# Kernel tuning notes

Measured on AMD Instinct MI355X. Metric: run time of the kernel, lower is better.

Reference implementation:

```python
import jax, jax.numpy as jnp
import numpy as np

N_NODES = 50000
N_EDGES = 1_600_000
IN_C, HID_C, OUT_C = 512, 256, 50
ALPHA = 0.1
NUM_LAYERS = 10


def setup_inputs() -> dict:
    key = jax.random.key(0)
    ks = jax.random.split(key, 8)
    x = jax.random.normal(ks[0], (N_NODES, IN_C), dtype=jnp.float32)
    edge_row = jax.random.randint(ks[1], (N_EDGES,), 0, N_NODES, dtype=jnp.int32)
    edge_col = jax.random.randint(ks[2], (N_EDGES,), 0, N_NODES, dtype=jnp.int32)
    edge_weight = jax.random.uniform(ks[3], (N_EDGES,), dtype=jnp.float32)
    s1 = 1.0 / np.sqrt(IN_C)
    s2 = 1.0 / np.sqrt(HID_C)
    W1 = jax.random.uniform(ks[4], (IN_C, HID_C), minval=-s1, maxval=s1, dtype=jnp.float32)
    b1 = jax.random.uniform(ks[5], (HID_C,), minval=-s1, maxval=s1, dtype=jnp.float32)
    W2 = jax.random.uniform(ks[6], (HID_C, OUT_C), minval=-s2, maxval=s2, dtype=jnp.float32)
    b2 = jax.random.uniform(ks[7], (OUT_C,), minval=-s2, maxval=s2, dtype=jnp.float32)
    return {"x": x, "edge_row": edge_row, "edge_col": edge_col,
            "edge_weight": edge_weight, "W1": W1, "b1": b1, "W2": W2, "b2": b2}


def reference(x, edge_row, edge_col, edge_weight, W1, b1, W2, b2):
    # MLP: Linear -> ReLU -> Linear (dropout inactive in eval, no batch norm)
    h = jax.nn.relu(x @ W1 + b1)          # [N, HID_C]
    h = h @ W2 + b2                        # [N, OUT_C]
    x0 = h

    def spmm(v):
        # out[i] = sum_{e: row[e]==i} w[e] * v[col[e]]
        msgs = v[edge_col] * edge_weight[:, None]   # [E, OUT_C]
        return jax.ops.segment_sum(msgs, edge_row, num_segments=N_NODES)

    def step(h, _):
        h = spmm(h) * (1.0 - ALPHA) + ALPHA * x0
        return h, None

    h, _ = jax.lax.scan(step, h, None, length=NUM_LAYERS)
    return jax.nn.log_softmax(h, axis=1)
```

## Files before the change

kernel.cpp:

```cpp
#include <hip/hip_runtime.h>
#include <cstddef>
#include <cstdint>
#include <math.h>

#define N_NODES 50000
#define N_EDGES 1600000
#define IN_C 512
#define HID_C 256
#define OUT_C 50
#define PAD_C 64
#define NUM_LAYERS 10
#define NBUCK 98
#define BSHIFT 9
#define BCAP 20480
#define PHB_CHUNK 8192
#define PHB_BLOCKS 196

typedef __attribute__((ext_vector_type(8))) short short8;
typedef __attribute__((ext_vector_type(4))) float floatx4;

__device__ inline unsigned short f2bf(float f) {
    unsigned int u = __float_as_uint(f);
    u += 0x7fffu + ((u >> 16) & 1u);
    return (unsigned short)(u >> 16);
}

#define ASYNC16(g, l)                                                     \
    __builtin_amdgcn_global_load_lds(                                     \
        (const __attribute__((address_space(1))) void*)(g),               \
        (__attribute__((address_space(3))) void*)(l), 16, 0, 0)

#define WAITCNT6() asm volatile("s_waitcnt vmcnt(6)" ::: "memory")
#define WAITCNT0() asm volatile("s_waitcnt vmcnt(0)" ::: "memory")
#define SBAR()     __builtin_amdgcn_s_barrier()
#define SFENCE()   __builtin_amdgcn_sched_barrier(0)

__global__ __launch_bounds__(256) void transpose_w1(const float* __restrict__ W1,
                                                    unsigned short* __restrict__ Wt) {
    __shared__ float tile[32][33];
    int bx = blockIdx.x;
    int by = blockIdx.y;
    int tx = threadIdx.x & 31, ty = threadIdx.x >> 5;
#pragma unroll
    for (int i = 0; i < 32; i += 8)
        tile[ty + i][tx] = W1[(bx * 32 + ty + i) * HID_C + by * 32 + tx];
    __syncthreads();
#pragma unroll
    for (int i = 0; i < 32; i += 8)
        Wt[(size_t)(by * 32 + ty + i) * IN_C + bx * 32 + tx] = f2bf(tile[tx][ty + i]);
}

__global__ void pad_w2(const float* __restrict__ W2, const float* __restrict__ b2,
                       unsigned short* __restrict__ Wpt, float* __restrict__ bp) {
    int idx = blockIdx.x * blockDim.x + threadIdx.x;
    if (idx < PAD_C * HID_C) {
        int n = idx >> 8, k = idx & 255;
        float v = (n < OUT_C) ? W2[k * OUT_C + n] : 0.f;
        Wpt[idx] = f2bf(v);
    }
    if (idx < PAD_C) bp[idx] = (idx < OUT_C) ? b2[idx] : 0.f;
}

__global__ __launch_bounds__(256) void gemm1_fused(const float* __restrict__ A,
                                                   const unsigned short* __restrict__ Wt,
                                                   const float* __restrict__ b1,
                                                   const unsigned short* __restrict__ Wpt,
                                                   const float* __restrict__ bp,
                                                   float* __restrict__ h0f,
                                                   unsigned short* __restrict__ h0b) {
    __shared__ __align__(16) char smem[49152];
    float*          As0 = (float*)smem;
    float*          As1 = (float*)(smem + 8192);
    unsigned short* Bs0 = (unsigned short*)(smem + 16384);
    unsigned short* Bs1 = (unsigned short*)(smem + 32768);
    unsigned short* Hs  = (unsigned short*)smem;
    const int HS_LD = 264;

    const int tid  = threadIdx.x;
    const int wave = tid >> 6, lane = tid & 63;
    const int quad = lane >> 4, l16 = lane & 15;
    const int m0 = blockIdx.x * 64;
    const int wm = (wave >> 1) * 32;
    const int wn = (wave & 1) * 128;

    floatx4 acc[2][8];
#pragma unroll
    for (int i = 0; i < 2; ++i)
#pragma unroll
        for (int j = 0; j < 8; ++j) acc[i][j] = (floatx4){0.f, 0.f, 0.f, 0.f};

    auto stage = [&](float* As_, unsigned short* Bs_, int k0) {
#pragma unroll
        for (int j = 0; j < 2; ++j) {
            int slot = tid + j * 256;
            int r = slot >> 3, c = slot & 7;
            int gr = m0 + r;
            if (gr >= N_NODES) gr = N_NODES - 1;
            const float* src = A + (size_t)gr * IN_C + k0 + ((c ^ (r & 7)) << 2);
            ASYNC16(src, As_ + (slot << 2));
        }
#pragma unroll
        for (int j = 0; j < 4; ++j) {
            const unsigned short* src = Wt + (size_t)tid * IN_C + k0 + (j << 3);
            ASYNC16(src, Bs_ + (j << 11) + (tid << 3));
        }
    };

    auto compute = [&](const float* As_, const unsigned short* Bs_) {
        short8 bfr[8], afr[2];
#pragma unroll
        for (int nt = 0; nt < 8; ++nt) {
            int n = wn + nt * 16 + l16;
            bfr[nt] = *(const short8*)&Bs_[(quad << 11) + (n << 3)];
        }
#pragma unroll
        for (int mt = 0; mt < 2; ++mt) {
            int r  = wm + mt * 16 + l16;
            int rx = r & 7;
            float4 lo = *(const float4*)&As_[(r << 5) + (((2 * quad)     ^ rx) << 2)];
            float4 hi = *(const float4*)&As_[(r << 5) + (((2 * quad + 1) ^ rx) << 2)];
            short8 a;
            a[0] = (short)f2bf(lo.x); a[1] = (short)f2bf(lo.y);
            a[2] = (short)f2bf(lo.z); a[3] = (short)f2bf(lo.w);
            a[4] = (short)f2bf(hi.x); a[5] = (short)f2bf(hi.y);
            a[6] = (short)f2bf(hi.z); a[7] = (short)f2bf(hi.w);
            afr[mt] = a;
        }
#pragma unroll
        for (int mt = 0; mt < 2; ++mt)
#pragma unroll
            for (int nt = 0; nt < 8; ++nt)
                acc[mt][nt] = __builtin_amdgcn_mfma_f32_16x16x32_bf16(afr[mt], bfr[nt],
                                                                      acc[mt][nt], 0, 0, 0);
    };

    stage(As0, Bs0, 0);
    stage(As1, Bs1, 32);
    WAITCNT6(); SFENCE(); SBAR(); SFENCE();
    for (int kk = 0; kk < 7; ++kk) {
        compute(As0, Bs0);
        SFENCE(); SBAR(); SFENCE();
        stage(As0, Bs0, (2 * kk + 2) * 32);
        WAITCNT6(); SFENCE(); SBAR(); SFENCE();
        compute(As1, Bs1);
        SFENCE(); SBAR(); SFENCE();
        stage(As1, Bs1, (2 * kk + 3) * 32);
        WAITCNT6(); SFENCE(); SBAR(); SFENCE();
    }
    compute(As0, Bs0);
    SFENCE(); SBAR(); SFENCE();
    WAITCNT0(); SFENCE(); SBAR(); SFENCE();
    compute(As1, Bs1);
    __syncthreads();

#pragma unroll
    for (int nt = 0; nt < 8; ++nt) {
        int n = wn + nt * 16 + l16;
        float bn = b1[n];
#pragma unroll
        for (int mt = 0; mt < 2; ++mt)
#pragma unroll
            for (int r = 0; r < 4; ++r) {
                float v = acc[mt][nt][r] + bn;
                v = v > 0.f ? v : 0.f;
                Hs[(wm + mt * 16 + quad * 4 + r) * HS_LD + n] = f2bf(v);
            }
    }
    __syncthreads();

    floatx4 acc2[4];
#pragma unroll
    for (int nt = 0; nt < 4; ++nt) acc2[nt] = (floatx4){0.f, 0.f, 0.f, 0.f};
    const int hrow = (wave << 4) + l16;
#pragma unroll
    for (int k2 = 0; k2 < 8; ++k2) {
        short8 haf = *(const short8*)&Hs[hrow * HS_LD + (k2 << 5) + (quad << 3)];
#pragma unroll
        for (int nt = 0; nt < 4; ++nt) {
            short8 bf = *(const short8*)&Wpt[(size_t)((nt << 4) + l16) * HID_C + (k2 << 5) + (quad << 3)];
            acc2[nt] = __builtin_amdgcn_mfma_f32_16x16x32_bf16(haf, bf, acc2[nt], 0, 0, 0);
        }
    }
#pragma unroll
    for (int nt = 0; nt < 4; ++nt) {
        int c = (nt << 4) + l16;
        float bn = bp[c];
#pragma unroll
        for (int r = 0; r < 4; ++r) {
            int row = m0 + (wave << 4) + (quad << 2) + r;
            if (row < N_NODES) {
                float v = acc2[nt][r] + bn;
                h0f[(size_t)row * PAD_C + c] = v;
                h0b[(size_t)row * PAD_C + c] = f2bf(v);
            }
        }
    }
}

__global__ __launch_bounds__(256) void bucket_scatter(const int* __restrict__ erow,
                                                      const int* __restrict__ ecol,
                                                      const float* __restrict__ ew,
                                                      int* __restrict__ bfill,
                                                      uint2* __restrict__ buckets) {
    __shared__ int lcnt[NBUCK];
    __shared__ int lbase[NBUCK];
    const int t = threadIdx.x;
    for (int b = t; b < NBUCK; b += 256) lcnt[b] = 0;
    __syncthreads();
    const int e0 = blockIdx.x * PHB_CHUNK;
    const int e1 = min(e0 + PHB_CHUNK, N_EDGES);
    for (int e = e0 + t; e < e1; e += 256)
        atomicAdd(&lcnt[erow[e] >> BSHIFT], 1);
    __syncthreads();
    for (int b = t; b < NBUCK; b += 256) {
        lbase[b] = atomicAdd(&bfill[b], lcnt[b]);
        lcnt[b] = 0;
    }
    __syncthreads();
    for (int e = e0 + t; e < e1; e += 256) {
        int r = erow[e];
        int b = r >> BSHIFT;
        int o = atomicAdd(&lcnt[b], 1);
        int idx = lbase[b] + o;
        if (idx < BCAP) {
            unsigned packed = ((unsigned)(r - (b << BSHIFT)) << 17) | (unsigned)ecol[e];
            buckets[(size_t)b * BCAP + idx] = make_uint2(packed, __float_as_uint(ew[e]));
        }
    }
}

__global__ __launch_bounds__(128) void bucket_scan(const int* __restrict__ bfill,
                                                   int* __restrict__ bbase,
                                                   int* __restrict__ rowptr) {
    __shared__ int sd[128];
    int t = threadIdx.x;
    int v = (t < NBUCK) ? min(bfill[t], BCAP) : 0;
    sd[t] = v;
    __syncthreads();
    for (int off = 1; off < 128; off <<= 1) {
        int x = (t >= off) ? sd[t - off] : 0;
        __syncthreads();
        sd[t] += x;
        __syncthreads();
    }
    if (t < NBUCK) bbase[t] = sd[t] - v;
    if (t == NBUCK - 1) {
        bbase[NBUCK] = sd[t];
        rowptr[N_NODES] = sd[t];
    }
}

__global__ __launch_bounds__(256) void bucket_csr(const uint2* __restrict__ buckets,
                                                  const int* __restrict__ bfill,
                                                  const int* __restrict__ bbase,
                                                  int* __restrict__ rowptr,
                                                  uint2* __restrict__ edges) {
    __shared__ int hist[512];
    __shared__ int excl[512];
    __shared__ int psum[256];
    const int b = blockIdx.x;
    const int t = threadIdx.x;
    const int n = min(bfill[b], BCAP);
    const uint2* bk = buckets + (size_t)b * BCAP;

    hist[t] = 0; hist[t + 256] = 0;
    __syncthreads();
    for (int i = t; i < n; i += 256)
        atomicAdd(&hist[bk[i].x >> 17], 1);
    __syncthreads();
    int a0 = hist[2 * t], a1 = hist[2 * t + 1];
    psum[t] = a0 + a1;
    __syncthreads();
    for (int off = 1; off < 256; off <<= 1) {
        int x = (t >= off) ? psum[t - off] : 0;
        __syncthreads();
        psum[t] += x;
        __syncthreads();
    }
    int pe = psum[t] - (a0 + a1);
    excl[2 * t] = pe;
    excl[2 * t + 1] = pe + a0;
    __syncthreads();
    const int base = bbase[b];
#pragma unroll
    for (int k = 0; k < 2; ++k) {
        int lr = t + k * 256;
        int r = (b << BSHIFT) + lr;
        if (r < N_NODES) rowptr[r] = base + excl[lr];
    }
    hist[t] = 0; hist[t + 256] = 0;
    __syncthreads();
    for (int i = t; i < n; i += 256) {
        uint2 ed = bk[i];
        int lr = ed.x >> 17;
        int pos = base + excl[lr] + atomicAdd(&hist[lr], 1);
        edges[pos] = make_uint2(ed.x & 0x1FFFFu, ed.y);
    }
}

template <bool LAST>
__global__ __launch_bounds__(256) void prop8(const int* __restrict__ rowptr,
                                             const uint2* __restrict__ edges,
                                             const unsigned short* __restrict__ hin,
                                             const float* __restrict__ h0f,
                                             unsigned short* __restrict__ hout_b,
                                             float* __restrict__ out_f) {
    int wid = (blockIdx.x * blockDim.x + threadIdx.x) >> 6;
    if (wid >= N_NODES) return;
    int lane = threadIdx.x & 63;
    int slot = lane >> 3;
    int lc   = lane & 7;
    int s = rowptr[wid], e = rowptr[wid + 1];

    float acc0[8], acc1[8];
#pragma unroll
    for (int k = 0; k < 8; ++k) { acc0[k] = 0.f; acc1[k] = 0.f; }

    int i = s;
    for (; i + 16 <= e; i += 16) {
        uint2 cw0 = edges[i + slot];
        uint2 cw1 = edges[i + 8 + slot];
        uint4 hv0 = *(const uint4*)((const char*)hin + ((size_t)cw0.x << 7) + lc * 16);
        uint4 hv1 = *(const uint4*)((const char*)hin + ((size_t)cw1.x << 7) + lc * 16);
        float w0 = __uint_as_float(cw0.y);
        float w1 = __uint_as_float(cw1.y);
        acc0[0] = fmaf(w0, __uint_as_float(hv0.x << 16),         acc0[0]);
        acc0[1] = fmaf(w0, __uint_as_float(hv0.x & 0xffff0000u), acc0[1]);
        acc0[2] = fmaf(w0, __uint_as_float(hv0.y << 16),         acc0[2]);
        acc0[3] = fmaf(w0, __uint_as_float(hv0.y & 0xffff0000u), acc0[3]);
        acc0[4] = fmaf(w0, __uint_as_float(hv0.z << 16),         acc0[4]);
        acc0[5] = fmaf(w0, __uint_as_float(hv0.z & 0xffff0000u), acc0[5]);
        acc0[6] = fmaf(w0, __uint_as_float(hv0.w << 16),         acc0[6]);
        acc0[7] = fmaf(w0, __uint_as_float(hv0.w & 0xffff0000u), acc0[7]);
        acc1[0] = fmaf(w1, __uint_as_float(hv1.x << 16),         acc1[0]);
        acc1[1] = fmaf(w1, __uint_as_float(hv1.x & 0xffff0000u), acc1[1]);
        acc1[2] = fmaf(w1, __uint_as_float(hv1.y << 16),         acc1[2]);
        acc1[3] = fmaf(w1, __uint_as_float(hv1.y & 0xffff0000u), acc1[3]);
        acc1[4] = fmaf(w1, __uint_as_float(hv1.z << 16),         acc1[4]);
        acc1[5] = fmaf(w1, __uint_as_float(hv1.z & 0xffff0000u), acc1[5]);
        acc1[6] = fmaf(w1, __uint_as_float(hv1.w << 16),         acc1[6]);
        acc1[7] = fmaf(w1, __uint_as_float(hv1.w & 0xffff0000u), acc1[7]);
    }
    for (; i < e; i += 8) {
        int idx = i + slot;
        uint2 cw = (idx < e) ? edges[idx] : make_uint2(0u, 0u);
        float w  = (idx < e) ? __uint_as_float(cw.y) : 0.f;
        uint4 hv = *(const uint4*)((const char*)hin + ((size_t)cw.x << 7) + lc * 16);
        acc0[0] = fmaf(w, __uint_as_float(hv.x << 16),         acc0[0]);
        acc0[1] = fmaf(w, __uint_as_float(hv.x & 0xffff0000u), acc0[1]);
        acc0[2] = fmaf(w, __uint_as_float(hv.y << 16),         acc0[2]);
        acc0[3] = fmaf(w, __uint_as_float(hv.y & 0xffff0000u), acc0[3]);
        acc0[4] = fmaf(w, __uint_as_float(hv.z << 16),         acc0[4]);
        acc0[5] = fmaf(w, __uint_as_float(hv.z & 0xffff0000u), acc0[5]);
        acc0[6] = fmaf(w, __uint_as_float(hv.w << 16),         acc0[6]);
        acc0[7] = fmaf(w, __uint_as_float(hv.w & 0xffff0000u), acc0[7]);
    }

    float r[8];
#pragma unroll
    for (int k = 0; k < 8; ++k) {
        float v = acc0[k] + acc1[k];
        v += __shfl_xor(v, 8, 64);
        v += __shfl_xor(v, 16, 64);
        v += __shfl_xor(v, 32, 64);
        r[k] = v;
    }

    size_t off = (size_t)wid * PAD_C + lc * 8;
    float4 h0a = *(const float4*)(h0f + off);
    float4 h0b4 = *(const float4*)(h0f + off + 4);
    r[0] = 0.9f * r[0] + 0.1f * h0a.x;  r[1] = 0.9f * r[1] + 0.1f * h0a.y;
    r[2] = 0.9f * r[2] + 0.1f * h0a.z;  r[3] = 0.9f * r[3] + 0.1f * h0a.w;
    r[4] = 0.9f * r[4] + 0.1f * h0b4.x; r[5] = 0.9f * r[5] + 0.1f * h0b4.y;
    r[6] = 0.9f * r[6] + 0.1f * h0b4.z; r[7] = 0.9f * r[7] + 0.1f * h0b4.w;

    if (!LAST) {
        if (slot == 0) {
            uint4 u;
            u.x = ((unsigned)f2bf(r[1]) << 16) | f2bf(r[0]);
            u.y = ((unsigned)f2bf(r[3]) << 16) | f2bf(r[2]);
            u.z = ((unsigned)f2bf(r[5]) << 16) | f2bf(r[4]);
            u.w = ((unsigned)f2bf(r[7]) << 16) | f2bf(r[6]);
            *(uint4*)((char*)hout_b + ((size_t)wid << 7) + lc * 16) = u;
        }
    } else {
        int ch0 = lc * 8;
        float m = -INFINITY;
#pragma unroll
        for (int k = 0; k < 8; ++k) if (ch0 + k < OUT_C) m = fmaxf(m, r[k]);
        m = fmaxf(m, __shfl_xor(m, 1, 64));
        m = fmaxf(m, __shfl_xor(m, 2, 64));
        m = fmaxf(m, __shfl_xor(m, 4, 64));
        float ss = 0.f;
#pragma unroll
        for (int k = 0; k < 8; ++k) if (ch0 + k < OUT_C) ss += __expf(r[k] - m);
        ss += __shfl_xor(ss, 1, 64);
        ss += __shfl_xor(ss, 2, 64);
        ss += __shfl_xor(ss, 4, 64);
        float lse = __logf(ss);
        if (slot == 0) {
#pragma unroll
            for (int k = 0; k < 8; ++k)
                if (ch0 + k < OUT_C)
                    out_f[(size_t)wid * OUT_C + ch0 + k] = (r[k] - m) - lse;
        }
    }
}

extern "C" void kernel_launch(void* const* d_in, const int* in_sizes, int n_in,
                              void* d_out, int out_size, void* d_ws, size_t ws_size,
                              hipStream_t stream) {
    const float* x    = (const float*)d_in[0];
    const int*   erow = (const int*)d_in[1];
    const int*   ecol = (const int*)d_in[2];
    const float* ew   = (const float*)d_in[3];
    const float* W1   = (const float*)d_in[4];
    const float* b1   = (const float*)d_in[5];
    const float* W2   = (const float*)d_in[6];
    const float* b2   = (const float*)d_in[7];
    float* out = (float*)d_out;

    char* p = (char*)d_ws;
    auto alloc = [&](size_t bytes) {
        char* r = p;
        p += (bytes + 255) & ~(size_t)255;
        return r;
    };
    char*  scratch = alloc((size_t)NBUCK * BCAP * 8);
    float* h0f    = (float*)alloc((size_t)N_NODES * PAD_C * 4);
    unsigned short* h0b = (unsigned short*)alloc((size_t)N_NODES * PAD_C * 2);
    uint2* edges  = (uint2*)alloc((size_t)N_EDGES * 8);
    int*   rowptr = (int*)alloc((size_t)(N_NODES + 1) * 4);
    int*   bfill  = (int*)alloc((size_t)NBUCK * 4);
    int*   bbase  = (int*)alloc((size_t)(NBUCK + 1) * 4);
    float* bp     = (float*)alloc((size_t)PAD_C * 4);
    unsigned short* Wt  = (unsigned short*)alloc((size_t)HID_C * IN_C * 2);
    unsigned short* Wpt = (unsigned short*)alloc((size_t)PAD_C * HID_C * 2);
    uint2* buckets = (uint2*)scratch;
    unsigned short* ha = (unsigned short*)scratch;
    unsigned short* hb = (unsigned short*)(scratch + (size_t)N_NODES * PAD_C * 2);

    hipMemsetAsync(bfill, 0, (size_t)NBUCK * 4, stream);

    bucket_scatter<<<PHB_BLOCKS, 256, 0, stream>>>(erow, ecol, ew, bfill, buckets);
    bucket_scan<<<1, 128, 0, stream>>>(bfill, bbase, rowptr);
    bucket_csr<<<NBUCK, 256, 0, stream>>>(buckets, bfill, bbase, rowptr, edges);

    transpose_w1<<<dim3(IN_C / 32, HID_C / 32), 256, 0, stream>>>(W1, Wt);
    pad_w2<<<(PAD_C * HID_C + 255) / 256, 256, 0, stream>>>(W2, b2, Wpt, bp);
    gemm1_fused<<<(N_NODES + 63) / 64, 256, 0, stream>>>(x, Wt, b1, Wpt, bp, h0f, h0b);

    const int prop_blocks = (N_NODES * 64 + 255) / 256;
    const unsigned short* cur = h0b;
    unsigned short* nxt = ha;
    for (int l = 0; l < NUM_LAYERS - 1; ++l) {
        prop8<false><<<prop_blocks, 256, 0, stream>>>(rowptr, edges, cur, h0f,
                                                      nxt, nullptr);
        const unsigned short* t = nxt;
        nxt = (nxt == ha) ? hb : ha;
        cur = t;
    }
    prop8<true><<<prop_blocks, 256, 0, stream>>>(rowptr, edges, cur, h0f,
                                                 nullptr, out);
}
```

Before: 631.8 us.

## Load GEMM A tiles directly to registers with packed bf16 cvt; deepen SpMM unroll

The first GEMM no longer stages fp32 A tiles through LDS. Each lane loads its own A fragment directly from global into registers, prefetched one step ahead, and converts it with the hardware v_cvt_pk_bf16_f32 instruction instead of software rounding. Only the bf16 W1 tiles stay double-buffered in LDS, with plain __syncthreads instead of hand-placed waitcnt fences. This cuts LDS traffic and conversion ALU work and shrinks shared memory, which may improve occupancy, but A loads are less coalesced (16 rows of 32B per quad) and may expose latency. The propagation kernel also gains a 32-edge unrolled loop that puts more gathers in flight.

Result: slower. 644.5 us (+2.0%).

```diff
diff --git a/kernel.cpp b/kernel.cpp
--- a/kernel.cpp
+++ b/kernel.cpp
@@ -25,15 +25,25 @@
     return (unsigned short)(u >> 16);
 }
 
+__device__ inline unsigned cvtpk(float lo, float hi) {
+    unsigned r;
+    asm("v_cvt_pk_bf16_f32 %0, %1, %2" : "=v"(r) : "v"(lo), "v"(hi));
+    return r;
+}
+
+__device__ inline short8 pack_bf16x8(float4 lo, float4 hi) {
+    union { unsigned u[4]; short8 s; } r;
+    r.u[0] = cvtpk(lo.x, lo.y);
+    r.u[1] = cvtpk(lo.z, lo.w);
+    r.u[2] = cvtpk(hi.x, hi.y);
+    r.u[3] = cvtpk(hi.z, hi.w);
+    return r.s;
+}
+
 #define ASYNC16(g, l)                                                     \
     __builtin_amdgcn_global_load_lds(                                     \
         (const __attribute__((address_space(1))) void*)(g),               \
         (__attribute__((address_space(3))) void*)(l), 16, 0, 0)
-
-#define WAITCNT6() asm volatile("s_waitcnt vmcnt(6)" ::: "memory")
-#define WAITCNT0() asm volatile("s_waitcnt vmcnt(0)" ::: "memory")
-#define SBAR()     __builtin_amdgcn_s_barrier()
-#define SFENCE()   __builtin_amdgcn_sched_barrier(0)
 
 __global__ __launch_bounds__(256) void transpose_w1(const float* __restrict__ W1,
                                                     unsigned short* __restrict__ Wt) {
@@ -68,11 +78,9 @@
                                                    const float* __restrict__ bp,
                                                    float* __restrict__ h0f,
                                                    unsigned short* __restrict__ h0b) {
-    __shared__ __align__(16) char smem[49152];
-    float*          As0 = (float*)smem;
-    float*          As1 = (float*)(smem + 8192);
-    unsigned short* Bs0 = (unsigned short*)(smem + 16384);
-    unsigned short* Bs1 = (unsigned short*)(smem + 32768);
+    __shared__ __align__(16) char smem[33792];
+    unsigned short* Bs0 = (unsigned short*)smem;
+    unsigned short* Bs1 = (unsigned short*)(smem + 16384);
     unsigned short* Hs  = (unsigned short*)smem;
     const int HS_LD = 264;
 
@@ -89,16 +97,14 @@
 #pragma unroll
         for (int j = 0; j < 8; ++j) acc[i][j] = (floatx4){0.f, 0.f, 0.f, 0.f};
 
-    auto stage = [&](float* As_, unsigned short* Bs_, int k0) {
-#pragma unroll
-        for (int j = 0; j < 2; ++j) {
-            int slot = tid + j * 256;
-            int r = slot >> 3, c = slot & 7;
-            int gr = m0 + r;
-            if (gr >= N_NODES) gr = N_NODES - 1;
-            const float* src = A + (size_t)gr * IN_C + k0 + ((c ^ (r & 7)) << 2);
-            ASYNC16(src, As_ + (slot << 2));
-        }
+    int r0 = m0 + wm + l16;
+    int r1 = r0 + 16;
+    if (r0 >= N_NODES) r0 = N_NODES - 1;
+    if (r1 >= N_NODES) r1 = N_NODES - 1;
+    const float* a0 = A + (size_t)r0 * IN_C + (quad << 3);
+    const float* a1 = A + (size_t)r1 * IN_C + (quad << 3);
+
+    auto stageB = [&](unsigned short* Bs_, int k0) {
 #pragma unroll
         for (int j = 0; j < 4; ++j) {
             const unsigned short* src = Wt + (size_t)tid * IN_C + k0 + (j << 3);
@@ -106,52 +112,46 @@
         }
     };
 
-    auto compute = [&](const float* As_, const unsigned short* Bs_) {
-        short8 bfr[8], afr[2];
+    float4 pa[4];
+    auto loadA = [&](int k0) {
+        pa[0] = *(const float4*)(a0 + k0);
+        pa[1] = *(const float4*)(a0 + k0 + 4);
+        pa[2] = *(const float4*)(a1 + k0);
+        pa[3] = *(const float4*)(a1 + k0 + 4);
+    };
+
+    auto compute = [&](const unsigned short* Bs_, short8 af0, short8 af1) {
 #pragma unroll
         for (int nt = 0; nt < 8; ++nt) {
-            int n = wn + nt * 16 + l16;
-            bfr[nt] = *(const short8*)&Bs_[(quad << 11) + (n << 3)];
-        }
-#pragma unroll
-        for (int mt = 0; mt < 2; ++mt) {
-            int r  = wm + mt * 16 + l16;
-            int rx = r & 7;
-            float4 lo = *(const float4*)&As_[(r << 5) + (((2 * quad)     ^ rx) << 2)];
-            float4 hi = *(const float4*)&As_[(r << 5) + (((2 * quad + 1) ^ rx) << 2)];
-            short8 a;
-            a[0] = (short)f2bf(lo.x); a[1] = (short)f2bf(lo.y);
-            a[2] = (short)f2bf(lo.z); a[3] = (short)f2bf(lo.w);
-            a[4] = (short)f2bf(hi.x); a[5] = (short)f2bf(hi.y);
-            a[6] = (short)f2bf(hi.z); a[7] = (short)f2bf(hi.w);
-            afr[mt] = a;
-        }
-#pragma unroll
-        for (int mt = 0; mt < 2; ++mt)
-#pragma unroll
-            for (int nt = 0; nt < 8; ++nt)
-                acc[mt][nt] = __builtin_amdgcn_mfma_f32_16x16x32_bf16(afr[mt], bfr[nt],
-                                                                      acc[mt][nt], 0, 0, 0);
+            short8 bf = *(const short8*)&Bs_[(quad << 11) + ((wn + nt * 16 + l16) << 3)];
+            acc[0][nt] = __builtin_amdgcn_mfma_f32_16x16x32_bf16(af0, bf, acc[0][nt], 0, 0, 0);
+            acc[1][nt] = __builtin_amdgcn_mfma_f32_16x16x32_bf16(af1, bf, acc[1][nt], 0, 0, 0);
+        }
     };
 
-    stage(As0, Bs0, 0);
-    stage(As1, Bs1, 32);
-    WAITCNT6(); SFENCE(); SBAR(); SFENCE();
-    for (int kk = 0; kk < 7; ++kk) {
-        compute(As0, Bs0);
-        SFENCE(); SBAR(); SFENCE();
-        stage(As0, Bs0, (2 * kk + 2) * 32);
-        WAITCNT6(); SFENCE(); SBAR(); SFENCE();
-        compute(As1, Bs1);
-        SFENCE(); SBAR(); SFENCE();
-        stage(As1, Bs1, (2 * kk + 3) * 32);
-        WAITCNT6(); SFENCE(); SBAR(); SFENCE();
-    }
-    compute(As0, Bs0);
-    SFENCE(); SBAR(); SFENCE();
-    WAITCNT0(); SFENCE(); SBAR(); SFENCE();
-    compute(As1, Bs1);
-    __syncthreads();
+    stageB(Bs0, 0);
+    loadA(0);
+    __syncthreads();
+
+    for (int kp = 0; kp < 8; ++kp) {
+        const int k0 = kp * 64;
+        stageB(Bs1, k0 + 32);
+        {
+            short8 af0 = pack_bf16x8(pa[0], pa[1]);
+            short8 af1 = pack_bf16x8(pa[2], pa[3]);
+            loadA(k0 + 32);
+            compute(Bs0, af0, af1);
+        }
+        __syncthreads();
+        if (kp < 7) stageB(Bs0, k0 + 64);
+        {
+            short8 af0 = pack_bf16x8(pa[0], pa[1]);
+            short8 af1 = pack_bf16x8(pa[2], pa[3]);
+            if (kp < 7) loadA(k0 + 64);
+            compute(Bs1, af0, af1);
+        }
+        __syncthreads();
+    }
 
 #pragma unroll
     for (int nt = 0; nt < 8; ++nt) {
@@ -296,6 +296,17 @@
         int pos = base + excl[lr] + atomicAdd(&hist[lr], 1);
         edges[pos] = make_uint2(ed.x & 0x1FFFFu, ed.y);
     }
+}
+
+__device__ inline void edge_fma(float* acc, float wgt, uint4 hv) {
+    acc[0] = fmaf(wgt, __uint_as_float(hv.x << 16),         acc[0]);
+    acc[1] = fmaf(wgt, __uint_as_float(hv.x & 0xffff0000u), acc[1]);
+    acc[2] = fmaf(wgt, __uint_as_float(hv.y << 16),         acc[2]);
+    acc[3] = fmaf(wgt, __uint_as_float(hv.y & 0xffff0000u), acc[3]);
+    acc[4] = fmaf(wgt, __uint_as_float(hv.z << 16),         acc[4]);
+    acc[5] = fmaf(wgt, __uint_as_float(hv.z & 0xffff0000u), acc[5]);
+    acc[6] = fmaf(wgt, __uint_as_float(hv.w << 16),         acc[6]);
+    acc[7] = fmaf(wgt, __uint_as_float(hv.w & 0xffff0000u), acc[7]);
 }
 
 template <bool LAST>
@@ -317,43 +328,34 @@
     for (int k = 0; k < 8; ++k) { acc0[k] = 0.f; acc1[k] = 0.f; }
 
     int i = s;
+    for (; i + 32 <= e; i += 32) {
+        uint2 cw0 = edges[i + slot];
+        uint2 cw1 = edges[i + 8 + slot];
+        uint2 cw2 = edges[i + 16 + slot];
+        uint2 cw3 = edges[i + 24 + slot];
+        uint4 hv0 = *(const uint4*)((const char*)hin + ((size_t)cw0.x << 7) + lc * 16);
+        uint4 hv1 = *(const uint4*)((const char*)hin + ((size_t)cw1.x << 7) + lc * 16);
+        uint4 hv2 = *(const uint4*)((const char*)hin + ((size_t)cw2.x << 7) + lc * 16);
+        uint4 hv3 = *(const uint4*)((const char*)hin + ((size_t)cw3.x << 7) + lc * 16);
+        edge_fma(acc0, __uint_as_float(cw0.y), hv0);
+        edge_fma(acc1, __uint_as_float(cw1.y), hv1);
+        edge_fma(acc0, __uint_as_float(cw2.y), hv2);
+        edge_fma(acc1, __uint_as_float(cw3.y), hv3);
+    }
     for (; i + 16 <= e; i += 16) {
         uint2 cw0 = edges[i + slot];
         uint2 cw1 = edges[i + 8 + slot];
         uint4 hv0 = *(const uint4*)((const char*)hin + ((size_t)cw0.x << 7) + lc * 16);
         uint4 hv1 = *(const uint4*)((const char*)hin + ((size_t)cw1.x << 7) + lc * 16);
-        float w0 = __uint_as_float(cw0.y);
-        float w1 = __uint_as_float(cw1.y);
-        acc0[0] = fmaf(w0, __uint_as_float(hv0.x << 16),         acc0[0]);
-        acc0[1] = fmaf(w0, __uint_as_float(hv0.x & 0xffff0000u), acc0[1]);
-        acc0[2] = fmaf(w0, __uint_as_float(hv0.y << 16),         acc0[2]);
-        acc0[3] = fmaf(w0, __uint_as_float(hv0.y & 0xffff0000u), acc0[3]);
-        acc0[4] = fmaf(w0, __uint_as_float(hv0.z << 16),         acc0[4]);
-        acc0[5] = fmaf(w0, __uint_as_float(hv0.z & 0xffff0000u), acc0[5]);
-        acc0[6] = fmaf(w0, __uint_as_float(hv0.w << 16),         acc0[6]);
-        acc0[7] = fmaf(w0, __uint_as_float(hv0.w & 0xffff0000u), acc0[7]);
-        acc1[0] = fmaf(w1, __uint_as_float(hv1.x << 16),         acc1[0]);
-        acc1[1] = fmaf(w1, __uint_as_float(hv1.x & 0xffff0000u), acc1[1]);
-        acc1[2] = fmaf(w1, __uint_as_float(hv1.y << 16),         acc1[2]);
-        acc1[3] = fmaf(w1, __uint_as_float(hv1.y & 0xffff0000u), acc1[3]);
-        acc1[4] = fmaf(w1, __uint_as_float(hv1.z << 16),         acc1[4]);
-        acc1[5] = fmaf(w1, __uint_as_float(hv1.z & 0xffff0000u), acc1[5]);
-        acc1[6] = fmaf(w1, __uint_as_float(hv1.w << 16),         acc1[6]);
-        acc1[7] = fmaf(w1, __uint_as_float(hv1.w & 0xffff0000u), acc1[7]);
+        edge_fma(acc0, __uint_as_float(cw0.y), hv0);
+        edge_fma(acc1, __uint_as_float(cw1.y), hv1);
     }
     for (; i < e; i += 8) {
         int idx = i + slot;
         uint2 cw = (idx < e) ? edges[idx] : make_uint2(0u, 0u);
-        float w  = (idx < e) ? __uint_as_float(cw.y) : 0.f;
+        float wgt = (idx < e) ? __uint_as_float(cw.y) : 0.f;
         uint4 hv = *(const uint4*)((const char*)hin + ((size_t)cw.x << 7) + lc * 16);
-        acc0[0] = fmaf(w, __uint_as_float(hv.x << 16),         acc0[0]);
-        acc0[1] = fmaf(w, __uint_as_float(hv.x & 0xffff0000u), acc0[1]);
-        acc0[2] = fmaf(w, __uint_as_float(hv.y << 16),         acc0[2]);
-        acc0[3] = fmaf(w, __uint_as_float(hv.y & 0xffff0000u), acc0[3]);
-        acc0[4] = fmaf(w, __uint_as_float(hv.z << 16),         acc0[4]);
-        acc0[5] = fmaf(w, __uint_as_float(hv.z & 0xffff0000u), acc0[5]);
-        acc0[6] = fmaf(w, __uint_as_float(hv.w << 16),         acc0[6]);
-        acc0[7] = fmaf(w, __uint_as_float(hv.w & 0xffff0000u), acc0[7]);
+        edge_fma(acc0, wgt, hv);
     }
 
     float r[8];
```
